# Kernel tuning notes

Hardware: AMD Instinct MI355X
Metric: run time of the kernel (lower is better)

Reference implementation:

```python
import jax, jax.numpy as jnp
import numpy as np

NUM_LAYERS = 3  # min_num_layers == max_num_layers == 3 (deterministic stochastic depth)
LN_EPS = 1e-5


def setup_inputs() -> dict:
    key = jax.random.key(0)
    k1, k2, k3 = jax.random.split(key, 3)
    N, d, F = 8, 16, 512  # (batch, in_dim=out_dim, num_features)
    x = jax.random.normal(k1, (N, d, F), dtype=jnp.float32)
    W = jax.random.normal(k2, (d, F, F, d), dtype=jnp.float32)  # recurrent weight
    A = jax.random.uniform(k3, (2, F, F), dtype=jnp.float32)    # transition mats, steps 1..2
    return {"x": x, "W": W, "A": A}


def _contract(h, W, a):
    # h: (N,d,F), W: (d,F,F,o), a: (F,F) -> (N,o,F)
    # Equivalent to (h.unsqueeze(-1).unsqueeze(-1) * (W * a[...,None])).sum(1).sum(1).transpose(1,2)
    return jnp.einsum('ndf,dfgo,fg->nog', h, W, a)


def _layer_norm(y):
    # torch applies layer_norm over the channel dim (axis 1 of (N,o,F)), no affine params
    m = y.mean(axis=1, keepdims=True)
    v = y.var(axis=1, keepdims=True)
    return (y - m) / jnp.sqrt(v + LN_EPS)


def reference(x, W, A):
    history = [x]
    for i in range(1, NUM_LAYERS):
        # recurrent + residual branch: average contributions from all previous layers
        ys = [_contract(history[j], W, A[i - j - 1]) for j in range(i)]
        y = jnp.mean(jnp.stack(ys, axis=0), axis=0)
        y = _layer_norm(y)
        history.append(y)
    return history[-1]  # return_layers='last'
```

## Files before the change

### kernel.cpp

```cpp
#include <hip/hip_runtime.h>
#include <stdint.h>


#define FC   32
#define NCH  16

template <bool SECOND>
__global__ __launch_bounds__(256)
void k_contract(const float* __restrict__ W, const float* __restrict__ A,
                const float* __restrict__ in,
                float* __restrict__ p0, float* __restrict__ p1) {
    __shared__ float sx[FC][16][8];
    __shared__ float sA0[FC][16];
    __shared__ float sA1[FC][16];

    const int t  = threadIdx.x;
    const int fc = blockIdx.x;
    const int ct = blockIdx.y;
    const int f0 = fc * FC;

    if constexpr (!SECOND) {
#pragma unroll
        for (int k = 0; k < 16; ++k) {
            int idx = k * 256 + t;
            int fl = idx >> 7, d = (idx >> 3) & 15, n = idx & 7;
            sx[fl][d][n] = in[n * 8192 + d * 512 + f0 + fl];
        }
    } else {
#pragma unroll
        for (int k = 0; k < 16; ++k) {
            int idx = k * 256 + t;
            int fl = idx >> 7, o = (idx >> 3) & 15, n = idx & 7;
            float s = 0.f;
#pragma unroll
            for (int ch = 0; ch < NCH; ++ch)
                s += in[(((size_t)ch * 512 + f0 + fl) * 16 + o) * 8 + n];
            sx[fl][o][n] = s;
        }
        __syncthreads();
        {
            int fl = t >> 3, n = t & 7;
            float m = 0.f, v = 0.f;
#pragma unroll
            for (int oo = 0; oo < 16; ++oo) { float y = sx[fl][oo][n]; m += y; v += y * y; }
            m *= (1.f / 16.f);
            v = v * (1.f / 16.f) - m * m;
            float r = rsqrtf(v + 1e-5f);
#pragma unroll
            for (int oo = 0; oo < 16; ++oo) sx[fl][oo][n] = (sx[fl][oo][n] - m) * r;
        }
    }
#pragma unroll
    for (int k = 0; k < 2; ++k) {
        int idx = k * 256 + t;
        int fl = idx >> 4, gl = idx & 15;
        sA0[fl][gl] = A[(size_t)(f0 + fl) * 512 + ct * 16 + gl];
        if constexpr (!SECOND)
            sA1[fl][gl] = A[262144 + (size_t)(f0 + fl) * 512 + ct * 16 + gl];
    }
    __syncthreads();

    const int gl  = t >> 4;
    const int col = ct * 256 + t;
    const float* Wc = W + col;

    float c0[8], c1[8];
#pragma unroll
    for (int n = 0; n < 8; ++n) { c0[n] = 0.f; c1[n] = 0.f; }

    for (int s = 0; s < FC; ++s) {
        const int fl = SECOND ? (FC - 1 - s) : s;
        const int f  = f0 + fl;

        float w[16];
#pragma unroll
        for (int d = 0; d < 16; ++d)
            w[d] = __builtin_nontemporal_load(Wc + (size_t)d * 4194304 + (size_t)f * 8192);

        float p[8];
#pragma unroll
        for (int n = 0; n < 8; ++n) p[n] = 0.f;
#pragma unroll
        for (int d = 0; d < 16; ++d) {
            float4 xa = *reinterpret_cast<const float4*>(&sx[fl][d][0]);
            float4 xb = *reinterpret_cast<const float4*>(&sx[fl][d][4]);
            p[0] = fmaf(xa.x, w[d], p[0]);
            p[1] = fmaf(xa.y, w[d], p[1]);
            p[2] = fmaf(xa.z, w[d], p[2]);
            p[3] = fmaf(xa.w, w[d], p[3]);
            p[4] = fmaf(xb.x, w[d], p[4]);
            p[5] = fmaf(xb.y, w[d], p[5]);
            p[6] = fmaf(xb.z, w[d], p[6]);
            p[7] = fmaf(xb.w, w[d], p[7]);
        }

        const float a0 = sA0[fl][gl];
#pragma unroll
        for (int n = 0; n < 8; ++n) c0[n] = fmaf(a0, p[n], c0[n]);
        if constexpr (!SECOND) {
            const float a1 = sA1[fl][gl];
#pragma unroll
            for (int n = 0; n < 8; ++n) c1[n] = fmaf(a1, p[n], c1[n]);
        }
    }

    size_t base = ((size_t)fc * 8192 + col) * 8;
    float4* dst0 = reinterpret_cast<float4*>(p0 + base);
    dst0[0] = make_float4(c0[0], c0[1], c0[2], c0[3]);
    dst0[1] = make_float4(c0[4], c0[5], c0[6], c0[7]);
    if constexpr (!SECOND) {
        float4* dst1 = reinterpret_cast<float4*>(p1 + base);
        dst1[0] = make_float4(c1[0], c1[1], c1[2], c1[3]);
        dst1[1] = make_float4(c1[4], c1[5], c1[6], c1[7]);
    }
}

__global__ __launch_bounds__(128)
void k_final(const float* __restrict__ p1, const float* __restrict__ p2,
             float* __restrict__ out) {
    __shared__ float sh[16][8];
    int g = blockIdx.x;
    int t = threadIdx.x;
    int o = t >> 3, n = t & 7;
    float s0 = 0.f, s1 = 0.f;
#pragma unroll
    for (int ch = 0; ch < NCH; ++ch) {
        size_t idx = (((size_t)ch * 512 + g) * 16 + o) * 8 + n;
        s0 += p1[idx];
        s1 += p2[idx];
    }
    float s = 0.5f * (s0 + s1);
    sh[o][n] = s;
    __syncthreads();
    float m = 0.f, v = 0.f;
#pragma unroll
    for (int oo = 0; oo < 16; ++oo) { float y = sh[oo][n]; m += y; v += y * y; }
    m *= (1.f / 16.f);
    v = v * (1.f / 16.f) - m * m;
    float r = rsqrtf(v + 1e-5f);
    out[n * 8192 + o * 512 + g] = (s - m) * r;
}

extern "C" void kernel_launch(void* const* d_in, const int* in_sizes, int n_in,
                              void* d_out, int out_size, void* d_ws, size_t ws_size,
                              hipStream_t stream) {
    const float* x = (const float*)d_in[0];
    const float* W = (const float*)d_in[1];
    const float* A = (const float*)d_in[2];
    float* out = (float*)d_out;

    float* ws  = (float*)d_ws;
    float* c0p = ws;
    float* c1p = c0p + 1048576;
    float* c2p = c1p + 1048576;

    k_contract<false><<<dim3(NCH, 32), 256, 0, stream>>>(W, A, x,   c0p, c1p);
    k_contract<true ><<<dim3(NCH, 32), 256, 0, stream>>>(W, A, c0p, c2p, nullptr);
    k_final<<<512, 128, 0, stream>>>(c1p, c2p, out);
}
```

Measured before the change: 410.7 us.

## Split f into more chunks and hoist layer-norm into a separate reduce kernel

Lowers the per-block f-chunk from 32 to 8 and raises the number of chunks from 16 to 64, so the grid has four times as many blocks to fill the GPU. The second contraction no longer reduces partials and runs layer-norm redundantly in every block. A new reduce+layernorm kernel does this once and writes a transposed normalized tensor that the second contraction loads with a single float4 copy. The cost is four times larger partial-sum buffers, more reduction traffic, and an extra kernel launch.

```diff
diff --git a/kernel.cpp b/kernel.cpp
--- a/kernel.cpp
+++ b/kernel.cpp
@@ -2,8 +2,8 @@
 #include <stdint.h>
 
 
-#define FC   32
-#define NCH  16
+#define FC   8
+#define NCH  64
 
 template <bool SECOND>
 __global__ __launch_bounds__(256)
@@ -21,39 +21,17 @@
 
     if constexpr (!SECOND) {
 #pragma unroll
-        for (int k = 0; k < 16; ++k) {
+        for (int k = 0; k < 4; ++k) {
             int idx = k * 256 + t;
             int fl = idx >> 7, d = (idx >> 3) & 15, n = idx & 7;
             sx[fl][d][n] = in[n * 8192 + d * 512 + f0 + fl];
         }
     } else {
-#pragma unroll
-        for (int k = 0; k < 16; ++k) {
-            int idx = k * 256 + t;
-            int fl = idx >> 7, o = (idx >> 3) & 15, n = idx & 7;
-            float s = 0.f;
-#pragma unroll
-            for (int ch = 0; ch < NCH; ++ch)
-                s += in[(((size_t)ch * 512 + f0 + fl) * 16 + o) * 8 + n];
-            sx[fl][o][n] = s;
-        }
-        __syncthreads();
-        {
-            int fl = t >> 3, n = t & 7;
-            float m = 0.f, v = 0.f;
-#pragma unroll
-            for (int oo = 0; oo < 16; ++oo) { float y = sx[fl][oo][n]; m += y; v += y * y; }
-            m *= (1.f / 16.f);
-            v = v * (1.f / 16.f) - m * m;
-            float r = rsqrtf(v + 1e-5f);
-#pragma unroll
-            for (int oo = 0; oo < 16; ++oo) sx[fl][oo][n] = (sx[fl][oo][n] - m) * r;
-        }
+        const float4* src = reinterpret_cast<const float4*>(in + (size_t)f0 * 128);
+        reinterpret_cast<float4*>(&sx[0][0][0])[t] = src[t];
     }
-#pragma unroll
-    for (int k = 0; k < 2; ++k) {
-        int idx = k * 256 + t;
-        int fl = idx >> 4, gl = idx & 15;
+    if (t < 128) {
+        int fl = t >> 4, gl = t & 15;
         sA0[fl][gl] = A[(size_t)(f0 + fl) * 512 + ct * 16 + gl];
         if constexpr (!SECOND)
             sA1[fl][gl] = A[262144 + (size_t)(f0 + fl) * 512 + ct * 16 + gl];
@@ -116,20 +94,49 @@
 }
 
 __global__ __launch_bounds__(128)
+void k_reduce_ln(const float* __restrict__ part, float* __restrict__ outT) {
+    __shared__ float sh[16][8];
+    int g = blockIdx.x;
+    int t = threadIdx.x;
+    int o = t >> 3, n = t & 7;
+    size_t base = ((size_t)g * 16 + o) * 8 + n;
+    float s0 = 0.f, s1 = 0.f, s2 = 0.f, s3 = 0.f;
+#pragma unroll
+    for (int ch = 0; ch < NCH; ch += 4) {
+        s0 += part[(size_t)(ch + 0) * 65536 + base];
+        s1 += part[(size_t)(ch + 1) * 65536 + base];
+        s2 += part[(size_t)(ch + 2) * 65536 + base];
+        s3 += part[(size_t)(ch + 3) * 65536 + base];
+    }
+    float s = (s0 + s1) + (s2 + s3);
+    sh[o][n] = s;
+    __syncthreads();
+    float m = 0.f, v = 0.f;
+#pragma unroll
+    for (int oo = 0; oo < 16; ++oo) { float y = sh[oo][n]; m += y; v += y * y; }
+    m *= (1.f / 16.f);
+    v = v * (1.f / 16.f) - m * m;
+    float r = rsqrtf(v + 1e-5f);
+    outT[base] = (s - m) * r;
+}
+
+__global__ __launch_bounds__(128)
 void k_final(const float* __restrict__ p1, const float* __restrict__ p2,
              float* __restrict__ out) {
     __shared__ float sh[16][8];
     int g = blockIdx.x;
     int t = threadIdx.x;
     int o = t >> 3, n = t & 7;
-    float s0 = 0.f, s1 = 0.f;
+    size_t base = (((size_t)g) * 16 + o) * 8 + n;
+    float s0 = 0.f, s1 = 0.f, s2 = 0.f, s3 = 0.f;
 #pragma unroll
-    for (int ch = 0; ch < NCH; ++ch) {
-        size_t idx = (((size_t)ch * 512 + g) * 16 + o) * 8 + n;
-        s0 += p1[idx];
-        s1 += p2[idx];
+    for (int ch = 0; ch < NCH; ch += 2) {
+        size_t i0 = (size_t)(ch + 0) * 65536 + base;
+        size_t i1 = (size_t)(ch + 1) * 65536 + base;
+        s0 += p1[i0]; s1 += p2[i0];
+        s2 += p1[i1]; s3 += p2[i1];
     }
-    float s = 0.5f * (s0 + s1);
+    float s = 0.5f * ((s0 + s1) + (s2 + s3));
     sh[o][n] = s;
     __syncthreads();
     float m = 0.f, v = 0.f;
@@ -151,10 +158,12 @@
 
     float* ws  = (float*)d_ws;
     float* c0p = ws;
-    float* c1p = c0p + 1048576;
-    float* c2p = c1p + 1048576;
+    float* c1p = c0p + 4194304;
+    float* c2p = c1p + 4194304;
+    float* h1T = c2p + 4194304;
 
     k_contract<false><<<dim3(NCH, 32), 256, 0, stream>>>(W, A, x,   c0p, c1p);
-    k_contract<true ><<<dim3(NCH, 32), 256, 0, stream>>>(W, A, c0p, c2p, nullptr);
+    k_reduce_ln<<<512, 128, 0, stream>>>(c0p, h1T);
+    k_contract<true ><<<dim3(NCH, 32), 256, 0, stream>>>(W, A, h1T, c2p, nullptr);
     k_final<<<512, 128, 0, stream>>>(c1p, c2p, out);
 }
```

New measurement: 415.2 us. About the same (+1.1%).
